# Performance work log

Measured on AMD Instinct MI355X. Metric: run time of the kernel, lower is better.

Reference implementation:

```python
import jax, jax.numpy as jnp
import numpy as np

EPS = 1e-5  # forward() default eps


def setup_inputs() -> dict:
    key = jax.random.key(0)
    k1, k2 = jax.random.split(key)
    x = jax.random.normal(k1, (16, 4, 1024, 1024), dtype=jnp.float32)
    hole = jax.random.uniform(k2, x.shape) < 0.3
    x = jnp.where(hole, 0.0, x)
    return {"x": x}


def reference(x):
    # mask_type='eq', mask_value=0: valid positions are x != 0
    valid = x != 0.0
    v = valid.astype(x.dtype)
    axes = (1, 2, 3)  # per-sample reduction over C,H,W (4D input skips per-channel branch)
    n = jnp.sum(v, axis=axes, keepdims=True)                       # [B,1,1,1] valid counts
    mean = jnp.sum(x * v, axis=axes, keepdims=True) / n            # masked mean
    centered = jnp.where(valid, x - mean, x)                       # masked-out entries unchanged
    # torch.var on the masked subset of the centered values: unbiased (ddof=1)
    m2 = jnp.sum(centered * v, axis=axes, keepdims=True) / n
    var = jnp.sum(v * (centered - m2) ** 2, axis=axes, keepdims=True) / (n - 1.0)
    out = jnp.where(valid, centered / (jnp.sqrt(var) + EPS), x)
    return out
```

## Files before the change

kernel.cpp:

```cpp
#include <hip/hip_runtime.h>


#define EPS 1e-5

constexpr int    B               = 16;
constexpr int    VEC_PER_SAMPLE  = 1048576;
constexpr int    RED_BLOCKS_PS   = 128;
constexpr int    RED_THREADS     = 256;
constexpr int    NORM_BLOCKS_PS  = 4096;
constexpr int    NORM_THREADS    = 256;

__device__ inline void wave_reduce(double& s1, double& s2, int& c) {
    #pragma unroll
    for (int off = 32; off > 0; off >>= 1) {
        s1 += __shfl_down(s1, off);
        s2 += __shfl_down(s2, off);
        c  += __shfl_down(c,  off);
    }
}

__global__ __launch_bounds__(RED_THREADS)
void masked_stats_kernel(const float4* __restrict__ x, double* __restrict__ ws) {
    const int sample = blockIdx.x / RED_BLOCKS_PS;
    const int blk    = blockIdx.x % RED_BLOCKS_PS;
    const float4* xs = x + (size_t)sample * VEC_PER_SAMPLE;

    double s1 = 0.0, s2 = 0.0;
    int cnt = 0;

    const int stride = RED_BLOCKS_PS * RED_THREADS;
    for (int i = blk * RED_THREADS + threadIdx.x; i < VEC_PER_SAMPLE; i += stride) {
        float4 v = xs[i];
        s1 += (double)v.x + (double)v.y + (double)v.z + (double)v.w;
        s2 += (double)v.x * v.x + (double)v.y * v.y
            + (double)v.z * v.z + (double)v.w * v.w;
        cnt += (v.x != 0.0f) + (v.y != 0.0f) + (v.z != 0.0f) + (v.w != 0.0f);
    }

    wave_reduce(s1, s2, cnt);

    __shared__ double L1[4], L2[4];
    __shared__ int    LC[4];
    const int wave = threadIdx.x >> 6;
    const int lane = threadIdx.x & 63;
    if (lane == 0) { L1[wave] = s1; L2[wave] = s2; LC[wave] = cnt; }
    __syncthreads();
    if (threadIdx.x == 0) {
        double t1 = 0.0, t2 = 0.0; int tc = 0;
        #pragma unroll
        for (int w = 0; w < 4; ++w) { t1 += L1[w]; t2 += L2[w]; tc += LC[w]; }
        atomicAdd(&ws[sample * 3 + 0], t1);
        atomicAdd(&ws[sample * 3 + 1], t2);
        atomicAdd(&ws[sample * 3 + 2], (double)tc);
    }
}

__global__ __launch_bounds__(NORM_THREADS)
void masked_norm_kernel(const float4* __restrict__ x, float4* __restrict__ out,
                        const double* __restrict__ ws) {
    const int sample = blockIdx.x >> 12;

    const double sum   = ws[sample * 3 + 0];
    const double sumsq = ws[sample * 3 + 1];
    const double n     = ws[sample * 3 + 2];
    const double mean  = sum / n;
    const double var   = (sumsq - sum * sum / n) / (n - 1.0);
    const float  inv   = (float)(1.0 / (sqrt(var) + EPS));
    const float  fmean = (float)mean;

    const size_t idx = (size_t)blockIdx.x * NORM_THREADS + threadIdx.x;
    float4 v = x[idx];
    float4 o;
    o.x = (v.x != 0.0f) ? (v.x - fmean) * inv : 0.0f;
    o.y = (v.y != 0.0f) ? (v.y - fmean) * inv : 0.0f;
    o.z = (v.z != 0.0f) ? (v.z - fmean) * inv : 0.0f;
    o.w = (v.w != 0.0f) ? (v.w - fmean) * inv : 0.0f;
    out[idx] = o;
}

extern "C" void kernel_launch(void* const* d_in, const int* in_sizes, int n_in,
                              void* d_out, int out_size, void* d_ws, size_t ws_size,
                              hipStream_t stream) {
    const float4* x   = (const float4*)d_in[0];
    float4*       out = (float4*)d_out;
    double*       ws  = (double*)d_ws;

    hipMemsetAsync(d_ws, 0, B * 3 * sizeof(double), stream);

    masked_stats_kernel<<<B * RED_BLOCKS_PS, RED_THREADS, 0, stream>>>(x, ws);
    masked_norm_kernel<<<B * NORM_BLOCKS_PS, NORM_THREADS, 0, stream>>>(x, out, ws);
}
```

Baseline: 494.2 us.

## Use fp32 partial sums, per-block partials with finalize kernel, nontemporal stores

The stats kernel now accumulates in fp32 with four independent accumulators over a contiguous chunk per block, converting to double only for the cross-thread reduction. It writes per-block partials instead of double atomics, which removes the memset. A small finalize kernel computes mean and inverse std once per sample, so the norm kernel no longer repeats that double-precision math in every block. The norm kernel processes four float4 per thread and uses nontemporal stores to reduce cache pollution. The fp32 accumulation over many elements risks some precision loss, and the extra kernel adds a launch.

```diff
diff --git a/kernel.cpp b/kernel.cpp
--- a/kernel.cpp
+++ b/kernel.cpp
@@ -3,90 +3,134 @@
 
 #define EPS 1e-5
 
-constexpr int    B               = 16;
-constexpr int    VEC_PER_SAMPLE  = 1048576;
-constexpr int    RED_BLOCKS_PS   = 128;
-constexpr int    RED_THREADS     = 256;
-constexpr int    NORM_BLOCKS_PS  = 4096;
-constexpr int    NORM_THREADS    = 256;
+typedef float v4f __attribute__((ext_vector_type(4)));
 
-__device__ inline void wave_reduce(double& s1, double& s2, int& c) {
+constexpr int B               = 16;
+constexpr int VEC_PER_SAMPLE  = 1 << 20;
+constexpr int RED_BLOCKS_PS   = 128;
+constexpr int RED_THREADS     = 256;
+constexpr int RED_VPT         = VEC_PER_SAMPLE / (RED_BLOCKS_PS * RED_THREADS);
+constexpr int NORM_THREADS    = 256;
+constexpr int NORM_VPT        = 4;
+constexpr int NORM_BLOCKS_PS  = VEC_PER_SAMPLE / (NORM_THREADS * NORM_VPT);
+
+constexpr size_t FIN_OFFSET = (size_t)B * RED_BLOCKS_PS * 3 * sizeof(double);
+
+__global__ __launch_bounds__(RED_THREADS)
+void masked_stats_kernel(const float4* __restrict__ x, double* __restrict__ part) {
+    const int sample = blockIdx.x / RED_BLOCKS_PS;
+    const int blk    = blockIdx.x % RED_BLOCKS_PS;
+    const float4* xs = x + (size_t)sample * VEC_PER_SAMPLE
+                         + (size_t)blk * (RED_THREADS * RED_VPT);
+
+    float s1[4] = {0.f, 0.f, 0.f, 0.f};
+    float s2[4] = {0.f, 0.f, 0.f, 0.f};
+    int   cn[4] = {0, 0, 0, 0};
+
+    for (int k = 0; k < RED_VPT; k += 4) {
+        #pragma unroll
+        for (int u = 0; u < 4; ++u) {
+            float4 v = xs[(k + u) * RED_THREADS + threadIdx.x];
+            s1[u] += (v.x + v.y) + (v.z + v.w);
+            s2[u] += v.x * v.x;
+            s2[u] += v.y * v.y;
+            s2[u] += v.z * v.z;
+            s2[u] += v.w * v.w;
+            cn[u] += (v.x != 0.0f) + (v.y != 0.0f) + (v.z != 0.0f) + (v.w != 0.0f);
+        }
+    }
+
+    double d1 = ((double)s1[0] + s1[1]) + ((double)s1[2] + s1[3]);
+    double d2 = ((double)s2[0] + s2[1]) + ((double)s2[2] + s2[3]);
+    int    ct = (cn[0] + cn[1]) + (cn[2] + cn[3]);
+
     #pragma unroll
     for (int off = 32; off > 0; off >>= 1) {
-        s1 += __shfl_down(s1, off);
-        s2 += __shfl_down(s2, off);
-        c  += __shfl_down(c,  off);
+        d1 += __shfl_down(d1, off);
+        d2 += __shfl_down(d2, off);
+        ct += __shfl_down(ct, off);
     }
-}
-
-__global__ __launch_bounds__(RED_THREADS)
-void masked_stats_kernel(const float4* __restrict__ x, double* __restrict__ ws) {
-    const int sample = blockIdx.x / RED_BLOCKS_PS;
-    const int blk    = blockIdx.x % RED_BLOCKS_PS;
-    const float4* xs = x + (size_t)sample * VEC_PER_SAMPLE;
-
-    double s1 = 0.0, s2 = 0.0;
-    int cnt = 0;
-
-    const int stride = RED_BLOCKS_PS * RED_THREADS;
-    for (int i = blk * RED_THREADS + threadIdx.x; i < VEC_PER_SAMPLE; i += stride) {
-        float4 v = xs[i];
-        s1 += (double)v.x + (double)v.y + (double)v.z + (double)v.w;
-        s2 += (double)v.x * v.x + (double)v.y * v.y
-            + (double)v.z * v.z + (double)v.w * v.w;
-        cnt += (v.x != 0.0f) + (v.y != 0.0f) + (v.z != 0.0f) + (v.w != 0.0f);
-    }
-
-    wave_reduce(s1, s2, cnt);
 
     __shared__ double L1[4], L2[4];
     __shared__ int    LC[4];
     const int wave = threadIdx.x >> 6;
-    const int lane = threadIdx.x & 63;
-    if (lane == 0) { L1[wave] = s1; L2[wave] = s2; LC[wave] = cnt; }
+    if ((threadIdx.x & 63) == 0) { L1[wave] = d1; L2[wave] = d2; LC[wave] = ct; }
     __syncthreads();
     if (threadIdx.x == 0) {
         double t1 = 0.0, t2 = 0.0; int tc = 0;
         #pragma unroll
         for (int w = 0; w < 4; ++w) { t1 += L1[w]; t2 += L2[w]; tc += LC[w]; }
-        atomicAdd(&ws[sample * 3 + 0], t1);
-        atomicAdd(&ws[sample * 3 + 1], t2);
-        atomicAdd(&ws[sample * 3 + 2], (double)tc);
+        part[(size_t)blockIdx.x * 3 + 0] = t1;
+        part[(size_t)blockIdx.x * 3 + 1] = t2;
+        part[(size_t)blockIdx.x * 3 + 2] = (double)tc;
+    }
+}
+
+__global__ __launch_bounds__(128)
+void finalize_stats_kernel(const double* __restrict__ part, float2* __restrict__ fin) {
+    const int sample = blockIdx.x;
+    const size_t p = ((size_t)sample * RED_BLOCKS_PS + threadIdx.x) * 3;
+    double d1 = part[p + 0];
+    double d2 = part[p + 1];
+    double dc = part[p + 2];
+
+    #pragma unroll
+    for (int off = 32; off > 0; off >>= 1) {
+        d1 += __shfl_down(d1, off);
+        d2 += __shfl_down(d2, off);
+        dc += __shfl_down(dc, off);
+    }
+
+    __shared__ double L1[2], L2[2], LC[2];
+    const int wave = threadIdx.x >> 6;
+    if ((threadIdx.x & 63) == 0) { L1[wave] = d1; L2[wave] = d2; LC[wave] = dc; }
+    __syncthreads();
+    if (threadIdx.x == 0) {
+        double S1 = L1[0] + L1[1];
+        double S2 = L2[0] + L2[1];
+        double n  = LC[0] + LC[1];
+        double mean = S1 / n;
+        double var  = (S2 - S1 * S1 / n) / (n - 1.0);
+        float2 mi;
+        mi.x = (float)mean;
+        mi.y = (float)(1.0 / (sqrt(var) + EPS));
+        fin[sample] = mi;
     }
 }
 
 __global__ __launch_bounds__(NORM_THREADS)
-void masked_norm_kernel(const float4* __restrict__ x, float4* __restrict__ out,
-                        const double* __restrict__ ws) {
-    const int sample = blockIdx.x >> 12;
+void masked_norm_kernel(const float4* __restrict__ x, v4f* __restrict__ out,
+                        const float2* __restrict__ fin) {
+    const int sample = blockIdx.x / NORM_BLOCKS_PS;
+    const int blk    = blockIdx.x % NORM_BLOCKS_PS;
+    const float2 mi  = fin[sample];
+    const float mean = mi.x, inv = mi.y;
 
-    const double sum   = ws[sample * 3 + 0];
-    const double sumsq = ws[sample * 3 + 1];
-    const double n     = ws[sample * 3 + 2];
-    const double mean  = sum / n;
-    const double var   = (sumsq - sum * sum / n) / (n - 1.0);
-    const float  inv   = (float)(1.0 / (sqrt(var) + EPS));
-    const float  fmean = (float)mean;
+    const size_t base = (size_t)sample * VEC_PER_SAMPLE
+                      + (size_t)blk * (NORM_THREADS * NORM_VPT);
 
-    const size_t idx = (size_t)blockIdx.x * NORM_THREADS + threadIdx.x;
-    float4 v = x[idx];
-    float4 o;
-    o.x = (v.x != 0.0f) ? (v.x - fmean) * inv : 0.0f;
-    o.y = (v.y != 0.0f) ? (v.y - fmean) * inv : 0.0f;
-    o.z = (v.z != 0.0f) ? (v.z - fmean) * inv : 0.0f;
-    o.w = (v.w != 0.0f) ? (v.w - fmean) * inv : 0.0f;
-    out[idx] = o;
+    #pragma unroll
+    for (int u = 0; u < NORM_VPT; ++u) {
+        const size_t idx = base + (size_t)u * NORM_THREADS + threadIdx.x;
+        float4 v = x[idx];
+        v4f o;
+        o.x = (v.x != 0.0f) ? (v.x - mean) * inv : 0.0f;
+        o.y = (v.y != 0.0f) ? (v.y - mean) * inv : 0.0f;
+        o.z = (v.z != 0.0f) ? (v.z - mean) * inv : 0.0f;
+        o.w = (v.w != 0.0f) ? (v.w - mean) * inv : 0.0f;
+        __builtin_nontemporal_store(o, &out[idx]);
+    }
 }
 
 extern "C" void kernel_launch(void* const* d_in, const int* in_sizes, int n_in,
                               void* d_out, int out_size, void* d_ws, size_t ws_size,
                               hipStream_t stream) {
-    const float4* x   = (const float4*)d_in[0];
-    float4*       out = (float4*)d_out;
-    double*       ws  = (double*)d_ws;
+    const float4* x    = (const float4*)d_in[0];
+    v4f*          out  = (v4f*)d_out;
+    double*       part = (double*)d_ws;
+    float2*       fin  = (float2*)((char*)d_ws + FIN_OFFSET);
 
-    hipMemsetAsync(d_ws, 0, B * 3 * sizeof(double), stream);
-
-    masked_stats_kernel<<<B * RED_BLOCKS_PS, RED_THREADS, 0, stream>>>(x, ws);
-    masked_norm_kernel<<<B * NORM_BLOCKS_PS, NORM_THREADS, 0, stream>>>(x, out, ws);
+    masked_stats_kernel<<<B * RED_BLOCKS_PS, RED_THREADS, 0, stream>>>(x, part);
+    finalize_stats_kernel<<<B, 128, 0, stream>>>(part, fin);
+    masked_norm_kernel<<<B * NORM_BLOCKS_PS, NORM_THREADS, 0, stream>>>(x, out, fin);
 }
```

Measured after the change: 473.9 us. -4.1%, faster.
